# Kernel optimization log

Measured on AMD Instinct MI355X. Metric: run time of the kernel, lower is better.

## Reference

```python
import jax, jax.numpy as jnp
import numpy as np

B, C, T, H, W = 2, 512, 4, 32, 32
NH = 8          # num_heads
GROUPS = 32     # GroupNorm groups
EPS = 1e-5      # GroupNorm eps (torch default)


def setup_inputs() -> dict:
    key = jax.random.key(0)
    k0, k1, k2 = jax.random.split(key, 3)
    s = 0.02
    return {
        "x": jax.random.normal(k0, (B, C, T, H, W), jnp.float32),
        "gn_w": jnp.ones((C,), jnp.float32),
        "gn_b": jnp.zeros((C,), jnp.float32),
        "qkv_w": jax.random.normal(k1, (3 * C, C), jnp.float32) * s,
        "qkv_b": jnp.zeros((3 * C,), jnp.float32),
        "out_w": jax.random.normal(k2, (C, C), jnp.float32) * s,
        "out_b": jnp.zeros((C,), jnp.float32),
    }


def reference(x, gn_w, gn_b, qkv_w, qkv_b, out_w, out_b):
    Bb, Cc, Tt, Hh, Ww = x.shape
    N = Tt * Hh * Ww
    hd = Cc // NH

    # GroupNorm(32, C): normalize over (C//G, T, H, W) per group, biased var
    xg = x.reshape(Bb, GROUPS, -1)
    mean = jnp.mean(xg, axis=-1, keepdims=True)
    var = jnp.var(xg, axis=-1, keepdims=True)
    h = ((xg - mean) * jax.lax.rsqrt(var + EPS)).reshape(Bb, Cc, N)
    h = h * gn_w[None, :, None] + gn_b[None, :, None]

    # 1x1 Conv3d qkv == per-token linear over channels
    qkv = jnp.einsum('oc,bcn->bon', qkv_w, h) + qkv_b[None, :, None]
    qkv = qkv.reshape(Bb, 3, NH, hd, N).transpose(1, 0, 2, 4, 3)  # [3,B,nh,N,hd]
    q, k, v = qkv[0], qkv[1], qkv[2]

    scale = 1.0 / np.sqrt(hd).astype(np.float32)
    attn = jax.nn.softmax(jnp.einsum('bhnd,bhmd->bhnm', q, k) * scale, axis=-1)
    o = jnp.einsum('bhnm,bhmd->bhnd', attn, v)  # [B,nh,N,hd]

    # Faithful to original: h.permute(1,2,0,3).reshape(B,C,T,H,W)
    o = o.transpose(1, 2, 0, 3).reshape(Bb, Cc, N)
    o = jnp.einsum('oc,bcn->bon', out_w, o) + out_b[None, :, None]
    return x + o.reshape(Bb, Cc, Tt, Hh, Ww)
```

## Files before the change

### kernel.cpp

```cpp
#include <hip/hip_runtime.h>
#include <stdint.h>

#define B_    2
#define C_    512
#define NH_   8
#define HD_   64
#define N_    4096
#define G_    32
#define K_    512
#define EPS_  1e-5f
#define QSCALE_ 0.18033688011112042f

typedef __bf16 bf16;
typedef __attribute__((ext_vector_type(8))) __bf16 bf16x8;
typedef __attribute__((ext_vector_type(4))) float f32x4;

__global__ __launch_bounds__(256) void cvt2_k(const float* __restrict__ s0,
                                              const float* __restrict__ s1,
                                              bf16* __restrict__ d0,
                                              bf16* __restrict__ d1, int n0) {
  const int i = blockIdx.x * 256 + threadIdx.x;
  const float* s = (i < n0) ? s0 : s1;
  bf16* d = (i < n0) ? d0 : d1;
  const int k = (i < n0) ? i : i - n0;
  f32x4 v = *reinterpret_cast<const f32x4*>(s + (size_t)k * 4);
  bf16 o[4] = {(bf16)v[0], (bf16)v[1], (bf16)v[2], (bf16)v[3]};
  *reinterpret_cast<uint64_t*>(d + (size_t)k * 4) = *reinterpret_cast<uint64_t*>(o);
}

__global__ __launch_bounds__(256) void gn_part_k(const float* __restrict__ x,
                                                 float* __restrict__ part) {
  const int bb = blockIdx.x;
  const float* p = x + (size_t)bb * 16384;
  const int t = threadIdx.x;
  float s1 = 0.f, s2 = 0.f;
  for (int i = 0; i < 16; ++i) {
    f32x4 v = *reinterpret_cast<const f32x4*>(p + (size_t)(i * 256 + t) * 4);
#pragma unroll
    for (int j = 0; j < 4; ++j) { float f = v[j]; s1 += f; s2 += f * f; }
  }
#pragma unroll
  for (int o = 32; o > 0; o >>= 1) { s1 += __shfl_down(s1, o); s2 += __shfl_down(s2, o); }
  __shared__ float a1[4], a2[4];
  if ((t & 63) == 0) { a1[t >> 6] = s1; a2[t >> 6] = s2; }
  __syncthreads();
  if (t == 0) {
    part[bb * 2]     = a1[0] + a1[1] + a1[2] + a1[3];
    part[bb * 2 + 1] = a2[0] + a2[1] + a2[2] + a2[3];
  }
}

__global__ __launch_bounds__(256) void gn_apply_k(const float* __restrict__ x,
                                                  const float* __restrict__ part,
                                                  const float* __restrict__ gw,
                                                  const float* __restrict__ gb,
                                                  bf16* __restrict__ hT) {
  __shared__ float tile[64][65];
  const int n0 = blockIdx.x * 64, c0 = blockIdx.y * 64, b = blockIdx.z;
  const int t = threadIdx.x;
  {
    const int cc = t >> 2;
    const int nn = (t & 3) * 16;
    const int c = c0 + cc;
    const int bg = b * G_ + (c >> 4);
    float s1 = 0.f, s2 = 0.f;
#pragma unroll
    for (int q = 0; q < 4; ++q) {
      s1 += part[(bg * 4 + q) * 2];
      s2 += part[(bg * 4 + q) * 2 + 1];
    }
    const float mean = s1 * (1.f / 65536.f);
    const float var  = s2 * (1.f / 65536.f) - mean * mean;
    const float rstd = rsqrtf(var + EPS_);
    const float sw = gw[c] * rstd;
    const float sb = gb[c] - mean * sw;
    const float* xp = x + ((size_t)(b * C_ + c)) * N_ + n0 + nn;
#pragma unroll
    for (int q = 0; q < 4; ++q) {
      f32x4 v = *reinterpret_cast<const f32x4*>(xp + q * 4);
#pragma unroll
      for (int j = 0; j < 4; ++j) tile[cc][nn + q * 4 + j] = v[j] * sw + sb;
    }
  }
  __syncthreads();
  {
    const int rn = t >> 2;
    const int ch = (t & 3) * 16;
    bf16* hp = hT + ((size_t)b * N_ + n0 + rn) * C_ + c0 + ch;
    bf16x8 o0, o1;
#pragma unroll
    for (int j = 0; j < 8; ++j) {
      o0[j] = (bf16)tile[ch + j][rn];
      o1[j] = (bf16)tile[ch + 8 + j][rn];
    }
    *reinterpret_cast<bf16x8*>(hp)     = o0;
    *reinterpret_cast<bf16x8*>(hp + 8) = o1;
  }
}

template <int EPI>
__global__ __launch_bounds__(256) void gemm_bt_k(const bf16* __restrict__ A,
                                                 const bf16* __restrict__ BT,
                                                 const float* __restrict__ bias,
                                                 bf16* __restrict__ out0,
                                                 bf16* __restrict__ out1,
                                                 bf16* __restrict__ out2,
                                                 float* __restrict__ outf,
                                                 const float* __restrict__ xres) {
  __shared__ __align__(16) bf16 As[128][72];
  __shared__ __align__(16) bf16 Bs[128][72];
  const int t = threadIdx.x;
  const int w = t >> 6, lane = t & 63;
  const int quad = lane >> 4, l15 = lane & 15;
  const int m0 = blockIdx.y * 128, n0 = blockIdx.x * 128, b = blockIdx.z;
  const bf16* Ab = A + (size_t)m0 * K_;
  const bf16* Bb = BT + ((size_t)b * N_ + n0) * K_;
  const int srow = t >> 1;
  const int sk = (t & 1) * 32;

  f32x4 acc[4][4] = {};

  for (int kc = 0; kc < K_ / 64; ++kc) {
    __syncthreads();
    {
      const bf16* ag = Ab + (size_t)srow * K_ + kc * 64 + sk;
      const bf16* bg = Bb + (size_t)srow * K_ + kc * 64 + sk;
#pragma unroll
      for (int c = 0; c < 4; ++c) {
        *reinterpret_cast<bf16x8*>(&As[srow][sk + c * 8]) = *reinterpret_cast<const bf16x8*>(ag + c * 8);
        *reinterpret_cast<bf16x8*>(&Bs[srow][sk + c * 8]) = *reinterpret_cast<const bf16x8*>(bg + c * 8);
      }
    }
    __syncthreads();
    bf16x8 af[4][2], bfv[4][2];
#pragma unroll
    for (int i = 0; i < 4; ++i) {
      af[i][0] = *reinterpret_cast<const bf16x8*>(&As[(w >> 1) * 64 + i * 16 + l15][quad * 8]);
      af[i][1] = *reinterpret_cast<const bf16x8*>(&As[(w >> 1) * 64 + i * 16 + l15][quad * 8 + 32]);
    }
#pragma unroll
    for (int j = 0; j < 4; ++j) {
      bfv[j][0] = *reinterpret_cast<const bf16x8*>(&Bs[(w & 1) * 64 + j * 16 + l15][quad * 8]);
      bfv[j][1] = *reinterpret_cast<const bf16x8*>(&Bs[(w & 1) * 64 + j * 16 + l15][quad * 8 + 32]);
    }
#pragma unroll
    for (int i = 0; i < 4; ++i)
#pragma unroll
      for (int j = 0; j < 4; ++j) {
        acc[i][j] = __builtin_amdgcn_mfma_f32_16x16x32_bf16(af[i][0], bfv[j][0], acc[i][j], 0, 0, 0);
        acc[i][j] = __builtin_amdgcn_mfma_f32_16x16x32_bf16(af[i][1], bfv[j][1], acc[i][j], 0, 0, 0);
      }
  }

  const int rowbase = m0 + (w >> 1) * 64;
  const int colbase = n0 + (w & 1) * 64;
  if (EPI == 0) {
    const int which = m0 >> 9;
    if (which < 2) {
      bf16* dst = (which == 0) ? out0 : out1;
      const float sc = (which == 0) ? (float)QSCALE_ : 1.0f;
#pragma unroll
      for (int i = 0; i < 4; ++i) {
        const int mbase = rowbase + i * 16 + quad * 4;
        const int head = (mbase >> 6) & 7, d0 = mbase & 63;
        float bi[4];
#pragma unroll
        for (int r = 0; r < 4; ++r) bi[r] = bias[mbase + r];
#pragma unroll
        for (int j = 0; j < 4; ++j) {
          const int n = colbase + j * 16 + l15;
          union { bf16 h[4]; uint64_t u; } pk;
#pragma unroll
          for (int r = 0; r < 4; ++r) pk.h[r] = (bf16)((acc[i][j][r] + bi[r]) * sc);
          *reinterpret_cast<uint64_t*>(dst + ((size_t)(b * NH_ + head) * N_ + n) * HD_ + d0) = pk.u;
        }
      }
    } else {
#pragma unroll
      for (int i = 0; i < 4; ++i) {
        const int mbase = rowbase + i * 16 + quad * 4;
        const int head = (mbase >> 6) & 7;
#pragma unroll
        for (int r = 0; r < 4; ++r) {
          const int d = (mbase + r) & 63;
          const float bi = bias[mbase + r];
#pragma unroll
          for (int j = 0; j < 4; ++j) {
            const int n = colbase + j * 16 + l15;
            out2[((size_t)(b * NH_ + head) * HD_ + d) * N_ + n] = (bf16)(acc[i][j][r] + bi);
          }
        }
      }
    }
  } else {
#pragma unroll
    for (int i = 0; i < 4; ++i) {
#pragma unroll
      for (int r = 0; r < 4; ++r) {
        const int m = rowbase + i * 16 + quad * 4 + r;
        const float bi = bias[m];
#pragma unroll
        for (int j = 0; j < 4; ++j) {
          const int n = colbase + j * 16 + l15;
          const size_t idx = ((size_t)(b * C_ + m)) * N_ + n;
          outf[idx] = acc[i][j][r] + bi + xres[idx];
        }
      }
    }
  }
}

__global__ __launch_bounds__(256) void attn_k(const bf16* __restrict__ qb,
                                              const bf16* __restrict__ kb,
                                              const bf16* __restrict__ vb,
                                              bf16* __restrict__ oT) {
  __shared__ __align__(16) char smem[27648];
  bf16* Ks = (bf16*)smem;
  bf16* Vs = (bf16*)(smem + 9216);
  bf16* Ps = (bf16*)(smem + 18432);
  bf16* Ot = (bf16*)smem;

  const int t = threadIdx.x;
  const int w = t >> 6, lane = t & 63, quad = lane >> 4, l15 = lane & 15;
  const int rblk = blockIdx.x;
  const int bh = blockIdx.y, head = bh & 7, b = bh >> 3;
  const int z = blockIdx.z;
  const int bd = z * 4 + w;
  const bf16* qh = qb + (size_t)bh * N_ * HD_;
  const bf16* kh = kb + (size_t)bh * N_ * HD_;
  const bf16* vh = vb + (size_t)bh * HD_ * N_;

  bf16x8 qa0, qa1;
  {
    const bf16* qp = qh + ((size_t)((bd * 16 + l15) * 32 + rblk)) * HD_ + quad * 8;
    qa0 = *reinterpret_cast<const bf16x8*>(qp);
    qa1 = *reinterpret_cast<const bf16x8*>(qp + 32);
  }

  f32x4 acc[4] = {};
  float lsum[4] = {};

  const int sr = t >> 3, sc = (t & 7) * 8;
  const int s0 = (sr & 3) * 16 + (sr >> 2);
  const int s1 = ((sr + 32) & 3) * 16 + ((sr + 32) >> 2);
  bf16* Pw = Ps + w * 16 * 72;

  for (int kt = 0; kt < N_ / 64; ++kt) {
    __syncthreads();
    {
      const bf16* kg = kh + ((size_t)kt * 64) * HD_;
      *reinterpret_cast<bf16x8*>(Ks + s0 * 72 + sc) =
          *reinterpret_cast<const bf16x8*>(kg + (size_t)sr * HD_ + sc);
      *reinterpret_cast<bf16x8*>(Ks + s1 * 72 + sc) =
          *reinterpret_cast<const bf16x8*>(kg + (size_t)(sr + 32) * HD_ + sc);
      const bf16* vg = vh + (size_t)kt * 64;
      *reinterpret_cast<bf16x8*>(Vs + sr * 72 + sc) =
          *reinterpret_cast<const bf16x8*>(vg + (size_t)sr * N_ + sc);
      *reinterpret_cast<bf16x8*>(Vs + (sr + 32) * 72 + sc) =
          *reinterpret_cast<const bf16x8*>(vg + (size_t)(sr + 32) * N_ + sc);
    }
    __syncthreads();

    bf16x8 kf0[4], kf1[4];
#pragma unroll
    for (int mt = 0; mt < 4; ++mt) {
      kf0[mt] = *reinterpret_cast<const bf16x8*>(Ks + (mt * 16 + l15) * 72 + quad * 8);
      kf1[mt] = *reinterpret_cast<const bf16x8*>(Ks + (mt * 16 + l15) * 72 + quad * 8 + 32);
    }
    f32x4 S[4];
#pragma unroll
    for (int mt = 0; mt < 4; ++mt) {
      f32x4 zz = {0.f, 0.f, 0.f, 0.f};
      zz = __builtin_amdgcn_mfma_f32_16x16x32_bf16(qa0, kf0[mt], zz, 0, 0, 0);
      S[mt] = __builtin_amdgcn_mfma_f32_16x16x32_bf16(qa1, kf1[mt], zz, 0, 0, 0);
    }
#pragma unroll
    for (int r = 0; r < 4; ++r) {
      float p0 = __builtin_amdgcn_exp2f(S[0][r]);
      float p1 = __builtin_amdgcn_exp2f(S[1][r]);
      float p2 = __builtin_amdgcn_exp2f(S[2][r]);
      float p3 = __builtin_amdgcn_exp2f(S[3][r]);
      lsum[r] += (p0 + p1) + (p2 + p3);
      union { bf16 h[4]; uint64_t u; } pk;
      pk.h[0] = (bf16)p0; pk.h[1] = (bf16)p1; pk.h[2] = (bf16)p2; pk.h[3] = (bf16)p3;
      *reinterpret_cast<uint64_t*>(Pw + (quad * 4 + r) * 72 + l15 * 4) = pk.u;
    }
    asm volatile("s_waitcnt lgkmcnt(0)" ::: "memory");
    bf16x8 pa0 = *reinterpret_cast<const bf16x8*>(Pw + l15 * 72 + quad * 8);
    bf16x8 pa1 = *reinterpret_cast<const bf16x8*>(Pw + l15 * 72 + quad * 8 + 32);
#pragma unroll
    for (int dt = 0; dt < 4; ++dt) {
      bf16x8 vf0 = *reinterpret_cast<const bf16x8*>(Vs + (dt * 16 + l15) * 72 + quad * 8);
      bf16x8 vf1 = *reinterpret_cast<const bf16x8*>(Vs + (dt * 16 + l15) * 72 + quad * 8 + 32);
      acc[dt] = __builtin_amdgcn_mfma_f32_16x16x32_bf16(pa0, vf0, acc[dt], 0, 0, 0);
      acc[dt] = __builtin_amdgcn_mfma_f32_16x16x32_bf16(pa1, vf1, acc[dt], 0, 0, 0);
    }
  }

  float inv[4];
#pragma unroll
  for (int r = 0; r < 4; ++r) {
    float l = lsum[r];
#pragma unroll
    for (int o = 1; o < 16; o <<= 1) l += __shfl_xor(l, o);
    inv[r] = 1.f / l;
  }

  __syncthreads();
#pragma unroll
  for (int dt = 0; dt < 4; ++dt) {
    union { bf16 h[4]; uint64_t u; } o4;
#pragma unroll
    for (int r = 0; r < 4; ++r) o4.h[r] = (bf16)(acc[dt][r] * inv[r]);
    *reinterpret_cast<uint64_t*>(Ot + (dt * 16 + l15) * 72 + w * 16 + quad * 4) = o4.u;
  }
  __syncthreads();
  {
    const int d = t >> 2, ic = (t & 3) * 16;
    bf16* op = oT + (size_t)(head >> 2) * N_ * C_ +
               ((size_t)(rblk * 128 + b * 64 + d)) * C_ + (head & 3) * 128 + z * 64 + ic;
    *reinterpret_cast<bf16x8*>(op)     = *reinterpret_cast<const bf16x8*>(Ot + d * 72 + ic);
    *reinterpret_cast<bf16x8*>(op + 8) = *reinterpret_cast<const bf16x8*>(Ot + d * 72 + ic + 8);
  }
}

extern "C" void kernel_launch(void* const* d_in, const int* in_sizes, int n_in,
                              void* d_out, int out_size, void* d_ws, size_t ws_size,
                              hipStream_t stream) {
  const float* x     = (const float*)d_in[0];
  const float* gn_w  = (const float*)d_in[1];
  const float* gn_b  = (const float*)d_in[2];
  const float* qkv_w = (const float*)d_in[3];
  const float* qkv_b = (const float*)d_in[4];
  const float* out_w = (const float*)d_in[5];
  const float* out_b = (const float*)d_in[6];
  float* out = (float*)d_out;

  char* ws = (char*)d_ws;
  const size_t SZ = (size_t)B_ * C_ * N_ * sizeof(bf16);
  float* part  = (float*)ws;
  bf16* hT    = (bf16*)(ws + 4096);
  bf16* qbuf  = (bf16*)(ws + 4096 + SZ);
  bf16* kbuf  = (bf16*)(ws + 4096 + 2 * SZ);
  bf16* vbuf  = (bf16*)(ws + 4096 + 3 * SZ);
  bf16* oT    = (bf16*)(ws + 4096 + 4 * SZ);
  bf16* qkvwb = (bf16*)(ws + 4096 + 5 * SZ);
  bf16* outwb = qkvwb + (size_t)3 * C_ * C_;

  cvt2_k<<<dim3(1024), dim3(256), 0, stream>>>(qkv_w, out_w, qkvwb, outwb, (3 * C_ * C_) / 4);
  gn_part_k<<<dim3(256), dim3(256), 0, stream>>>(x, part);
  gn_apply_k<<<dim3(N_ / 64, C_ / 64, B_), dim3(256), 0, stream>>>(x, part, gn_w, gn_b, hT);
  gemm_bt_k<0><<<dim3(N_ / 128, (3 * C_) / 128, B_), dim3(256), 0, stream>>>(
      qkvwb, hT, qkv_b, qbuf, kbuf, vbuf, nullptr, nullptr);
  attn_k<<<dim3(32, B_ * NH_, 2), dim3(256), 0, stream>>>(qbuf, kbuf, vbuf, oT);
  gemm_bt_k<1><<<dim3(N_ / 128, C_ / 128, B_), dim3(256), 0, stream>>>(
      outwb, oT, out_b, nullptr, nullptr, nullptr, out, x);
}
```

Baseline: 249.7 us.

## Double-buffer K/V tiles in attention with 512-thread blocks and merge prep kernels

The attention kernel now uses 512-thread blocks covering 128 query rows. Each K/V tile is shared by twice as many waves, so K/V global loads are halved. K/V tiles are double-buffered in shared memory: the next tile is loaded into registers while the current one is processed, leaving one barrier per iteration instead of two. The weight-conversion and GroupNorm partial-sum kernels are merged into one launch to cut launch overhead. In exchange, shared memory per block doubles, the grid halves to 512 blocks, and register pressure may rise.

```diff
diff --git a/kernel.cpp b/kernel.cpp
--- a/kernel.cpp
+++ b/kernel.cpp
@@ -15,38 +15,41 @@
 typedef __attribute__((ext_vector_type(8))) __bf16 bf16x8;
 typedef __attribute__((ext_vector_type(4))) float f32x4;
 
-__global__ __launch_bounds__(256) void cvt2_k(const float* __restrict__ s0,
-                                              const float* __restrict__ s1,
-                                              bf16* __restrict__ d0,
-                                              bf16* __restrict__ d1, int n0) {
-  const int i = blockIdx.x * 256 + threadIdx.x;
-  const float* s = (i < n0) ? s0 : s1;
-  bf16* d = (i < n0) ? d0 : d1;
-  const int k = (i < n0) ? i : i - n0;
-  f32x4 v = *reinterpret_cast<const f32x4*>(s + (size_t)k * 4);
-  bf16 o[4] = {(bf16)v[0], (bf16)v[1], (bf16)v[2], (bf16)v[3]};
-  *reinterpret_cast<uint64_t*>(d + (size_t)k * 4) = *reinterpret_cast<uint64_t*>(o);
-}
-
-__global__ __launch_bounds__(256) void gn_part_k(const float* __restrict__ x,
-                                                 float* __restrict__ part) {
-  const int bb = blockIdx.x;
-  const float* p = x + (size_t)bb * 16384;
+__global__ __launch_bounds__(256) void prep_k(const float* __restrict__ qkv_w,
+                                              const float* __restrict__ out_w,
+                                              const float* __restrict__ x,
+                                              bf16* __restrict__ qkvwb,
+                                              bf16* __restrict__ outwb,
+                                              float* __restrict__ part) {
+  const int blk = blockIdx.x;
   const int t = threadIdx.x;
-  float s1 = 0.f, s2 = 0.f;
-  for (int i = 0; i < 16; ++i) {
-    f32x4 v = *reinterpret_cast<const f32x4*>(p + (size_t)(i * 256 + t) * 4);
-#pragma unroll
-    for (int j = 0; j < 4; ++j) { float f = v[j]; s1 += f; s2 += f * f; }
-  }
-#pragma unroll
-  for (int o = 32; o > 0; o >>= 1) { s1 += __shfl_down(s1, o); s2 += __shfl_down(s2, o); }
-  __shared__ float a1[4], a2[4];
-  if ((t & 63) == 0) { a1[t >> 6] = s1; a2[t >> 6] = s2; }
-  __syncthreads();
-  if (t == 0) {
-    part[bb * 2]     = a1[0] + a1[1] + a1[2] + a1[3];
-    part[bb * 2 + 1] = a2[0] + a2[1] + a2[2] + a2[3];
+  if (blk < 1024) {
+    const int i = blk * 256 + t;
+    const int n0 = (3 * C_ * C_) / 4;
+    const float* s = (i < n0) ? qkv_w : out_w;
+    bf16* d = (i < n0) ? qkvwb : outwb;
+    const int k = (i < n0) ? i : i - n0;
+    f32x4 v = *reinterpret_cast<const f32x4*>(s + (size_t)k * 4);
+    bf16 o[4] = {(bf16)v[0], (bf16)v[1], (bf16)v[2], (bf16)v[3]};
+    *reinterpret_cast<uint64_t*>(d + (size_t)k * 4) = *reinterpret_cast<uint64_t*>(o);
+  } else {
+    const int bb = blk - 1024;
+    const float* p = x + (size_t)bb * 16384;
+    float s1 = 0.f, s2 = 0.f;
+    for (int i = 0; i < 16; ++i) {
+      f32x4 v = *reinterpret_cast<const f32x4*>(p + (size_t)(i * 256 + t) * 4);
+#pragma unroll
+      for (int j = 0; j < 4; ++j) { float f = v[j]; s1 += f; s2 += f * f; }
+    }
+#pragma unroll
+    for (int o = 32; o > 0; o >>= 1) { s1 += __shfl_down(s1, o); s2 += __shfl_down(s2, o); }
+    __shared__ float a1[4], a2[4];
+    if ((t & 63) == 0) { a1[t >> 6] = s1; a2[t >> 6] = s2; }
+    __syncthreads();
+    if (t == 0) {
+      part[bb * 2]     = a1[0] + a1[1] + a1[2] + a1[3];
+      part[bb * 2 + 1] = a2[0] + a2[1] + a2[2] + a2[3];
+    }
   }
 }
 
@@ -210,29 +213,25 @@
   }
 }
 
-__global__ __launch_bounds__(256) void attn_k(const bf16* __restrict__ qb,
-                                              const bf16* __restrict__ kb,
-                                              const bf16* __restrict__ vb,
-                                              bf16* __restrict__ oT) {
-  __shared__ __align__(16) char smem[27648];
-  bf16* Ks = (bf16*)smem;
-  bf16* Vs = (bf16*)(smem + 9216);
-  bf16* Ps = (bf16*)(smem + 18432);
+__global__ __launch_bounds__(512, 4) void attn_k(const bf16* __restrict__ qb,
+                                                 const bf16* __restrict__ kb,
+                                                 const bf16* __restrict__ vb,
+                                                 bf16* __restrict__ oT) {
+  __shared__ __align__(16) char smem[55296];
+  bf16* Ps = (bf16*)(smem + 36864);
   bf16* Ot = (bf16*)smem;
 
   const int t = threadIdx.x;
   const int w = t >> 6, lane = t & 63, quad = lane >> 4, l15 = lane & 15;
   const int rblk = blockIdx.x;
   const int bh = blockIdx.y, head = bh & 7, b = bh >> 3;
-  const int z = blockIdx.z;
-  const int bd = z * 4 + w;
   const bf16* qh = qb + (size_t)bh * N_ * HD_;
   const bf16* kh = kb + (size_t)bh * N_ * HD_;
   const bf16* vh = vb + (size_t)bh * HD_ * N_;
 
   bf16x8 qa0, qa1;
   {
-    const bf16* qp = qh + ((size_t)((bd * 16 + l15) * 32 + rblk)) * HD_ + quad * 8;
+    const bf16* qp = qh + ((size_t)((w * 16 + l15) * 32 + rblk)) * HD_ + quad * 8;
     qa0 = *reinterpret_cast<const bf16x8*>(qp);
     qa1 = *reinterpret_cast<const bf16x8*>(qp + 32);
   }
@@ -240,32 +239,34 @@
   f32x4 acc[4] = {};
   float lsum[4] = {};
 
-  const int sr = t >> 3, sc = (t & 7) * 8;
-  const int s0 = (sr & 3) * 16 + (sr >> 2);
-  const int s1 = ((sr + 32) & 3) * 16 + ((sr + 32) >> 2);
+  const int j = t >> 3;
+  const int c8 = (t & 7) * 8;
+  const int pj = (j & 3) * 16 + (j >> 2);
   bf16* Pw = Ps + w * 16 * 72;
 
-  for (int kt = 0; kt < N_ / 64; ++kt) {
-    __syncthreads();
-    {
-      const bf16* kg = kh + ((size_t)kt * 64) * HD_;
-      *reinterpret_cast<bf16x8*>(Ks + s0 * 72 + sc) =
-          *reinterpret_cast<const bf16x8*>(kg + (size_t)sr * HD_ + sc);
-      *reinterpret_cast<bf16x8*>(Ks + s1 * 72 + sc) =
-          *reinterpret_cast<const bf16x8*>(kg + (size_t)(sr + 32) * HD_ + sc);
-      const bf16* vg = vh + (size_t)kt * 64;
-      *reinterpret_cast<bf16x8*>(Vs + sr * 72 + sc) =
-          *reinterpret_cast<const bf16x8*>(vg + (size_t)sr * N_ + sc);
-      *reinterpret_cast<bf16x8*>(Vs + (sr + 32) * 72 + sc) =
-          *reinterpret_cast<const bf16x8*>(vg + (size_t)(sr + 32) * N_ + sc);
-    }
-    __syncthreads();
+  {
+    bf16x8 kr = *reinterpret_cast<const bf16x8*>(kh + (size_t)j * HD_ + c8);
+    bf16x8 vr = *reinterpret_cast<const bf16x8*>(vh + (size_t)j * N_ + c8);
+    *reinterpret_cast<bf16x8*>((bf16*)smem + pj * 72 + c8) = kr;
+    *reinterpret_cast<bf16x8*>((bf16*)(smem + 9216) + j * 72 + c8) = vr;
+  }
+  __syncthreads();
+
+  for (int kt = 0; kt < 64; ++kt) {
+    bf16* curK = (bf16*)(smem + (kt & 1) * 18432);
+    bf16* curV = (bf16*)(smem + (kt & 1) * 18432 + 9216);
+
+    bf16x8 kr, vr;
+    if (kt != 63) {
+      kr = *reinterpret_cast<const bf16x8*>(kh + ((size_t)(kt + 1) * 64 + j) * HD_ + c8);
+      vr = *reinterpret_cast<const bf16x8*>(vh + (size_t)j * N_ + (kt + 1) * 64 + c8);
+    }
 
     bf16x8 kf0[4], kf1[4];
 #pragma unroll
     for (int mt = 0; mt < 4; ++mt) {
-      kf0[mt] = *reinterpret_cast<const bf16x8*>(Ks + (mt * 16 + l15) * 72 + quad * 8);
-      kf1[mt] = *reinterpret_cast<const bf16x8*>(Ks + (mt * 16 + l15) * 72 + quad * 8 + 32);
+      kf0[mt] = *reinterpret_cast<const bf16x8*>(curK + (mt * 16 + l15) * 72 + quad * 8);
+      kf1[mt] = *reinterpret_cast<const bf16x8*>(curK + (mt * 16 + l15) * 72 + quad * 8 + 32);
     }
     f32x4 S[4];
 #pragma unroll
@@ -290,11 +291,19 @@
     bf16x8 pa1 = *reinterpret_cast<const bf16x8*>(Pw + l15 * 72 + quad * 8 + 32);
 #pragma unroll
     for (int dt = 0; dt < 4; ++dt) {
-      bf16x8 vf0 = *reinterpret_cast<const bf16x8*>(Vs + (dt * 16 + l15) * 72 + quad * 8);
-      bf16x8 vf1 = *reinterpret_cast<const bf16x8*>(Vs + (dt * 16 + l15) * 72 + quad * 8 + 32);
+      bf16x8 vf0 = *reinterpret_cast<const bf16x8*>(curV + (dt * 16 + l15) * 72 + quad * 8);
+      bf16x8 vf1 = *reinterpret_cast<const bf16x8*>(curV + (dt * 16 + l15) * 72 + quad * 8 + 32);
       acc[dt] = __builtin_amdgcn_mfma_f32_16x16x32_bf16(pa0, vf0, acc[dt], 0, 0, 0);
       acc[dt] = __builtin_amdgcn_mfma_f32_16x16x32_bf16(pa1, vf1, acc[dt], 0, 0, 0);
     }
+
+    if (kt != 63) {
+      bf16* nK = (bf16*)(smem + ((kt + 1) & 1) * 18432);
+      bf16* nV = (bf16*)(smem + ((kt + 1) & 1) * 18432 + 9216);
+      *reinterpret_cast<bf16x8*>(nK + pj * 72 + c8) = kr;
+      *reinterpret_cast<bf16x8*>(nV + j * 72 + c8) = vr;
+    }
+    __syncthreads();
   }
 
   float inv[4];
@@ -306,21 +315,20 @@
     inv[r] = 1.f / l;
   }
 
-  __syncthreads();
 #pragma unroll
   for (int dt = 0; dt < 4; ++dt) {
     union { bf16 h[4]; uint64_t u; } o4;
 #pragma unroll
     for (int r = 0; r < 4; ++r) o4.h[r] = (bf16)(acc[dt][r] * inv[r]);
-    *reinterpret_cast<uint64_t*>(Ot + (dt * 16 + l15) * 72 + w * 16 + quad * 4) = o4.u;
+    *reinterpret_cast<uint64_t*>(Ot + (dt * 16 + l15) * 136 + w * 16 + quad * 4) = o4.u;
   }
   __syncthreads();
   {
-    const int d = t >> 2, ic = (t & 3) * 16;
+    const int d = t >> 3, ic = (t & 7) * 16;
     bf16* op = oT + (size_t)(head >> 2) * N_ * C_ +
-               ((size_t)(rblk * 128 + b * 64 + d)) * C_ + (head & 3) * 128 + z * 64 + ic;
-    *reinterpret_cast<bf16x8*>(op)     = *reinterpret_cast<const bf16x8*>(Ot + d * 72 + ic);
-    *reinterpret_cast<bf16x8*>(op + 8) = *reinterpret_cast<const bf16x8*>(Ot + d * 72 + ic + 8);
+               ((size_t)(rblk * 128 + b * 64 + d)) * C_ + (head & 3) * 128 + ic;
+    *reinterpret_cast<bf16x8*>(op)     = *reinterpret_cast<const bf16x8*>(Ot + d * 136 + ic);
+    *reinterpret_cast<bf16x8*>(op + 8) = *reinterpret_cast<const bf16x8*>(Ot + d * 136 + ic + 8);
   }
 }
 
@@ -347,12 +355,11 @@
   bf16* qkvwb = (bf16*)(ws + 4096 + 5 * SZ);
   bf16* outwb = qkvwb + (size_t)3 * C_ * C_;
 
-  cvt2_k<<<dim3(1024), dim3(256), 0, stream>>>(qkv_w, out_w, qkvwb, outwb, (3 * C_ * C_) / 4);
-  gn_part_k<<<dim3(256), dim3(256), 0, stream>>>(x, part);
+  prep_k<<<dim3(1280), dim3(256), 0, stream>>>(qkv_w, out_w, x, qkvwb, outwb, part);
   gn_apply_k<<<dim3(N_ / 64, C_ / 64, B_), dim3(256), 0, stream>>>(x, part, gn_w, gn_b, hT);
   gemm_bt_k<0><<<dim3(N_ / 128, (3 * C_) / 128, B_), dim3(256), 0, stream>>>(
       qkvwb, hT, qkv_b, qbuf, kbuf, vbuf, nullptr, nullptr);
-  attn_k<<<dim3(32, B_ * NH_, 2), dim3(256), 0, stream>>>(qbuf, kbuf, vbuf, oT);
+  attn_k<<<dim3(32, B_ * NH_), dim3(512), 0, stream>>>(qbuf, kbuf, vbuf, oT);
   gemm_bt_k<1><<<dim3(N_ / 128, C_ / 128, B_), dim3(256), 0, stream>>>(
       outwb, oT, out_b, nullptr, nullptr, nullptr, out, x);
 }
```

After: 224.1 us. 1.11x faster.
